# Kernel tuning notes

Measured on AMD Instinct MI355X. Metric: run time of the kernel, lower is better.

Reference implementation:

```python
import jax, jax.numpy as jnp
import numpy as np

HIDDEN = 4096
N_HEADS = 32
N_KV_HEADS = 8
HEAD_DIM = HIDDEN // N_HEADS  # 128
N_GROUPS = N_HEADS // N_KV_HEADS  # 4
ROPE_THETA = 10000.0
BSZ, SEQ = 2, 2048


def rotate_half(x):
    x1 = x[..., : x.shape[-1] // 2]
    x2 = x[..., x.shape[-1] // 2 :]
    return jnp.concatenate((-x2, x1), axis=-1)


def rope_tables(seq_len, head_dim, theta):
    inv_freq = 1.0 / theta ** (jnp.arange(0, head_dim, 2, dtype=jnp.float32) / head_dim)
    t = jnp.arange(seq_len, dtype=jnp.float32)
    freqs = jnp.einsum('i,j->ij', t, inv_freq)          # [S, head_dim/2]
    emb = jnp.concatenate((freqs, freqs), axis=-1)       # [S, head_dim]
    return jnp.cos(emb), jnp.sin(emb)


def setup_inputs() -> dict:
    key = jax.random.key(0)
    ks = jax.random.split(key, 5)
    hidden_states = jax.random.normal(ks[0], (BSZ, SEQ, HIDDEN), dtype=jnp.float32)
    # causal additive mask [B, 1, Q, K]
    causal = jnp.tril(jnp.ones((SEQ, SEQ), dtype=bool))
    attention_mask = jnp.where(causal, 0.0, -1e9).astype(jnp.float32)
    attention_mask = jnp.broadcast_to(attention_mask[None, None], (BSZ, 1, SEQ, SEQ))
    position_ids = jnp.broadcast_to(jnp.arange(SEQ, dtype=jnp.int32)[None, :], (BSZ, SEQ))
    sc = 1.0 / np.sqrt(HIDDEN)
    Wq = jax.random.normal(ks[1], (HIDDEN, N_HEADS * HEAD_DIM), dtype=jnp.float32) * sc
    Wk = jax.random.normal(ks[2], (HIDDEN, N_KV_HEADS * HEAD_DIM), dtype=jnp.float32) * sc
    Wv = jax.random.normal(ks[3], (HIDDEN, N_KV_HEADS * HEAD_DIM), dtype=jnp.float32) * sc
    Wo = jax.random.normal(ks[4], (N_HEADS * HEAD_DIM, HIDDEN), dtype=jnp.float32) * sc
    return {
        'hidden_states': hidden_states,
        'attention_mask': attention_mask,
        'position_ids': position_ids,
        'Wq': Wq, 'Wk': Wk, 'Wv': Wv, 'Wo': Wo,
    }


def reference(hidden_states, attention_mask, position_ids, Wq, Wk, Wv, Wo):
    bsz, q_len, _ = hidden_states.shape
    # QKV projections
    q = (hidden_states @ Wq).reshape(bsz, q_len, N_HEADS, HEAD_DIM).swapaxes(1, 2)       # [B,H,S,D]
    k = (hidden_states @ Wk).reshape(bsz, q_len, N_KV_HEADS, HEAD_DIM).swapaxes(1, 2)    # [B,Hkv,S,D]
    v = (hidden_states @ Wv).reshape(bsz, q_len, N_KV_HEADS, HEAD_DIM).swapaxes(1, 2)    # [B,Hkv,S,D]
    # RoPE
    cos_t, sin_t = rope_tables(q_len, HEAD_DIM, ROPE_THETA)
    cos = jnp.take(cos_t, position_ids, axis=0)[:, None]  # [B,1,S,D]
    sin = jnp.take(sin_t, position_ids, axis=0)[:, None]
    q = q * cos + rotate_half(q) * sin
    k = k * cos + rotate_half(k) * sin
    # GQA attention via grouped einsum (equivalent to repeat_kv, without materializing repeats)
    qg = q.reshape(bsz, N_KV_HEADS, N_GROUPS, q_len, HEAD_DIM)
    scores = jnp.einsum('bhgqd,bhkd->bhgqk', qg, k) / jnp.sqrt(jnp.float32(HEAD_DIM))
    scores = scores + attention_mask[:, :, None]  # broadcast mask over (kv_head, group)
    probs = jax.nn.softmax(scores.astype(jnp.float32), axis=-1).astype(hidden_states.dtype)
    out = jnp.einsum('bhgqk,bhkd->bhgqd', probs, v)
    out = out.reshape(bsz, N_HEADS, q_len, HEAD_DIM).swapaxes(1, 2).reshape(bsz, q_len, HIDDEN)
    return out @ Wo
```

## Files before the change

### kernel.cpp

```cpp
#include <hip/hip_runtime.h>
#include <hip/hip_bf16.h>
#include <cstdint>

#define HIDDEN 4096
#define NH 32
#define NKV 8
#define HD 128
#define SEQ 2048
#define BSZ 2
#define QKVN 6144
#define QKVLD 6144

using bf16x8 = __attribute__((ext_vector_type(8))) short;
using f32x4  = __attribute__((ext_vector_type(4))) float;

__device__ __forceinline__ ushort f2bf(float f) {
  union { float f; uint32_t u; } v; v.f = f;
  uint32_t r = (v.u + 0x7FFFu + ((v.u >> 16) & 1u)) >> 16;
  return (ushort)r;
}
__device__ __forceinline__ float bf2f(ushort s) {
  union { uint32_t u; float f; } v; v.u = ((uint32_t)s) << 16;
  return v.f;
}

__device__ __forceinline__ void gload_lds16(const void* g, void* l) {
  __builtin_amdgcn_global_load_lds(
      (const __attribute__((address_space(1))) void*)g,
      (__attribute__((address_space(3))) void*)l, 16, 0, 0);
}

__global__ __launch_bounds__(256)
void cvt_bf16_kernel(const float* __restrict__ X, ushort* __restrict__ Xb, int n8) {
  int t = blockIdx.x * 256 + threadIdx.x;
  if (t >= n8) return;
  size_t i = (size_t)t * 8;
  float4 a = *(const float4*)(X + i);
  float4 b = *(const float4*)(X + i + 4);
  uint4 p;
  p.x = (uint)f2bf(a.x) | ((uint)f2bf(a.y) << 16);
  p.y = (uint)f2bf(a.z) | ((uint)f2bf(a.w) << 16);
  p.z = (uint)f2bf(b.x) | ((uint)f2bf(b.y) << 16);
  p.w = (uint)f2bf(b.z) | ((uint)f2bf(b.w) << 16);
  *(uint4*)(Xb + i) = p;
}

__global__ __launch_bounds__(256)
void transpose_bf16_kernel(const float* __restrict__ W, ushort* __restrict__ WT,
                           int K, int N) {
  __shared__ ushort tile[32][33];
  const int k0 = blockIdx.y * 32, n0 = blockIdx.x * 32;
  const int tx = threadIdx.x & 31, ty = threadIdx.x >> 5;
  for (int i = 0; i < 4; ++i) {
    int k = ty + i * 8;
    tile[k][tx] = f2bf(W[(size_t)(k0 + k) * N + n0 + tx]);
  }
  __syncthreads();
  for (int i = 0; i < 4; ++i) {
    int n = ty + i * 8;
    WT[(size_t)(n0 + n) * K + k0 + tx] = tile[tx][n];
  }
}

__global__ __launch_bounds__(256)
void transpose_v_kernel(const ushort* __restrict__ Vsrc, ushort* __restrict__ VtG) {
  __shared__ ushort tile[32][33];
  const int slice = blockIdx.z;
  const int b = slice >> 3, kh = slice & 7;
  const int s0 = blockIdx.x * 32, d0 = blockIdx.y * 32;
  const int tx = threadIdx.x & 31, ty = threadIdx.x >> 5;
  const ushort* src = Vsrc + ((size_t)(b * SEQ) + s0) * QKVLD + kh * HD + d0;
  for (int i = 0; i < 4; ++i) {
    int s = ty + i * 8;
    tile[s][tx] = src[(size_t)s * QKVLD + tx];
  }
  __syncthreads();
  ushort* dst = VtG + ((size_t)slice * HD + d0) * SEQ + s0;
  for (int i = 0; i < 4; ++i) {
    int d = ty + i * 8;
    dst[(size_t)d * SEQ + tx] = tile[tx][d];
  }
}

template<int OUT_BF16>
__global__ __launch_bounds__(512, 2)
void gemm8p_kernel(const ushort* __restrict__ A, const ushort* __restrict__ BT,
                   void* __restrict__ Cp, int M, int N, int K) {
  extern __shared__ ushort lds[];
  const int tid = threadIdx.x, lane = tid & 63, wave = tid >> 6;
  const int l15 = lane & 15, l4 = lane >> 4;
  const int wr = wave >> 2, wc = wave & 3;

  const int mt = M >> 8, nt = N >> 8, nwg = mt * nt;
  const int swq = nwg >> 3, swr = nwg & 7;
  const int xcd = blockIdx.x & 7, lo = blockIdx.x >> 3;
  const int wg = (xcd < swr ? xcd * (swq + 1) : swr * (swq + 1) + (xcd - swr) * swq) + lo;
  const int m0 = (wg % mt) << 8;
  const int n0 = (wg / mt) << 8;

  ushort* LA[2][2];
  ushort* LB[2][2];
#pragma unroll
  for (int b_ = 0; b_ < 2; ++b_)
#pragma unroll
    for (int s_ = 0; s_ < 2; ++s_) {
      LA[b_][s_] = lds + ((b_ * 2 + 0) * 2 + s_) * 8192;
      LB[b_][s_] = lds + ((b_ * 2 + 1) * 2 + s_) * 8192;
    }

  const ushort* Abase = A + (size_t)m0 * K;
  const ushort* Bbase = BT + (size_t)n0 * K;

  const int srow0 = tid >> 2;
  const int scol8 = (((tid & 3) ^ ((srow0 >> 1) & 3)) << 3);

  const int swb  = (l4 ^ ((l15 >> 1) & 3)) << 3;
  const int aoff = (wr * 128 + l15) * 32 + swb;
  const int boff = (wc * 64 + l15) * 32 + swb;

  f32x4 acc[8][4] = {};
  bf16x8 a[8];
  bf16x8 b[4];

#define STAGE(buf, ks, kt, part)                                              \
  do {                                                                        \
    const size_t gc_ = (size_t)(kt) * 64 + (ks) * 32 + scol8;                 \
    const int rw_ = srow0 + (part) * 128;                                     \
    const int dst_ = ((part) * 512 + tid) * 8;                                \
    gload_lds16(Abase + (size_t)rw_ * K + gc_, &LA[buf][ks][dst_]);           \
    gload_lds16(Bbase + (size_t)rw_ * K + gc_, &LB[buf][ks][dst_]);           \
  } while (0)

#define MFMA_ __builtin_amdgcn_mfma_f32_16x16x32_bf16

#define PHASE_EVEN(buf, ks, sb, sk, skt)                                      \
  {                                                                           \
    _Pragma("unroll") for (int m_ = 0; m_ < 8; ++m_)                          \
      a[m_] = *(const bf16x8*)&LA[buf][ks][aoff + m_ * 512];                  \
    b[0] = *(const bf16x8*)&LB[buf][ks][boff];                                \
    b[1] = *(const bf16x8*)&LB[buf][ks][boff + 512];                          \
    STAGE(sb, sk, skt, 0);                                                    \
    asm volatile("s_barrier" ::: "memory");                                   \
    __builtin_amdgcn_s_setprio(1);                                            \
    _Pragma("unroll") for (int m_ = 0; m_ < 8; ++m_) {                        \
      acc[m_][0] = MFMA_(a[m_], b[0], acc[m_][0], 0, 0, 0);                   \
      acc[m_][1] = MFMA_(a[m_], b[1], acc[m_][1], 0, 0, 0);                   \
    }                                                                         \
    __builtin_amdgcn_s_setprio(0);                                            \
    asm volatile("s_barrier" ::: "memory");                                   \
  }

#define PHASE_ODD(buf, ks, sb, sk, skt)                                       \
  {                                                                           \
    b[2] = *(const bf16x8*)&LB[buf][ks][boff + 1024];                         \
    b[3] = *(const bf16x8*)&LB[buf][ks][boff + 1536];                         \
    STAGE(sb, sk, skt, 1);                                                    \
    asm volatile("s_barrier" ::: "memory");                                   \
    __builtin_amdgcn_s_setprio(1);                                            \
    _Pragma("unroll") for (int m_ = 0; m_ < 8; ++m_) {                        \
      acc[m_][2] = MFMA_(a[m_], b[2], acc[m_][2], 0, 0, 0);                   \
      acc[m_][3] = MFMA_(a[m_], b[3], acc[m_][3], 0, 0, 0);                   \
    }                                                                         \
    __builtin_amdgcn_s_setprio(0);                                            \
    asm volatile("s_waitcnt vmcnt(8)");                                       \
    asm volatile("s_barrier" ::: "memory");                                   \
  }

  const int NT = K >> 6;

  STAGE(0, 0, 0, 0); STAGE(0, 0, 0, 1);
  STAGE(0, 1, 0, 0); STAGE(0, 1, 0, 1);
  STAGE(1, 0, 1, 0); STAGE(1, 0, 1, 1);
  asm volatile("s_waitcnt vmcnt(8)");
  asm volatile("s_barrier" ::: "memory");

  for (int i = 0; i < (NT >> 1); ++i) {
    const int kt0 = 2 * i;
    const int ktA = (kt0 + 2 < NT) ? kt0 + 2 : NT - 1;
    const int ktB = (kt0 + 3 < NT) ? kt0 + 3 : NT - 1;
    PHASE_EVEN(0, 0, 1, 1, kt0 + 1)
    PHASE_ODD (0, 0, 1, 1, kt0 + 1)
    PHASE_EVEN(0, 1, 0, 0, ktA)
    PHASE_ODD (0, 1, 0, 0, ktA)
    PHASE_EVEN(1, 0, 0, 1, ktA)
    PHASE_ODD (1, 0, 0, 1, ktA)
    PHASE_EVEN(1, 1, 1, 0, ktB)
    PHASE_ODD (1, 1, 1, 0, ktB)
  }
#undef PHASE_EVEN
#undef PHASE_ODD
#undef STAGE

  const int crow0 = m0 + wr * 128 + l4 * 4;
  const int ccol0 = n0 + wc * 64 + l15;
#pragma unroll
  for (int m_ = 0; m_ < 8; ++m_)
#pragma unroll
    for (int n_ = 0; n_ < 4; ++n_)
#pragma unroll
      for (int r_ = 0; r_ < 4; ++r_) {
        const size_t row = crow0 + m_ * 16 + r_;
        const int col = ccol0 + n_ * 16;
        const float val = acc[m_][n_][r_];
        if (OUT_BF16) ((ushort*)Cp)[row * N + col] = f2bf(val);
        else          ((float*)Cp)[row * N + col]  = val;
      }
}

__global__ __launch_bounds__(256)
void rope_kernel(ushort* buf, const int* __restrict__ pos_ids, int nh, int ld, int total) {
  int t = blockIdx.x * 256 + threadIdx.x;
  if (t >= total) return;
  int j = t & 63;
  int rest = t >> 6;
  int h = rest % nh;
  int bs = rest / nh;
  float pos = (float)pos_ids[bs];
  float inv = exp2f(-(float)j * (13.287712379549449f / 64.0f));
  float ang = pos * inv;
  float c = cosf(ang), s = sinf(ang);
  ushort* p = buf + (size_t)bs * ld + h * HD + j;
  float x1 = bf2f(p[0]), x2 = bf2f(p[64]);
  p[0]  = f2bf(x1 * c - x2 * s);
  p[64] = f2bf(x2 * c + x1 * s);
}

__global__ __launch_bounds__(256)
void attn_kernel(const ushort* __restrict__ Q, const ushort* __restrict__ K0,
                 const ushort* __restrict__ VtG, ushort* __restrict__ AO) {
  __shared__ ushort Ks[64 * 128];
  __shared__ ushort Vs[2][128 * 64];
  __shared__ ushort Ps[4][32 * 72];

  const int raw  = blockIdx.x;
  const int kh   = raw & 7;
  const int rest = raw >> 3;
  const int qt   = 63 - (rest & 63);
  const int b    = rest >> 6;
  const int q0   = qt * 32;

  const int tid = threadIdx.x, lane = tid & 63, wave = tid >> 6;
  const int l15 = lane & 15, l4 = lane >> 4;
  const int h = kh * 4 + wave;
  const float SCL2 = 0.1275173110f;

  const size_t bS = (size_t)b * SEQ;
  const ushort* Kb = K0 + bS * QKVLD + kh * HD;
  const ushort* Vb = VtG + (size_t)(b * NKV + kh) * HD * SEQ;

  const int vrow = lane >> 3;
  const int vslot = lane & 7;

  bf16x8 qf[2][4];
#pragma unroll
  for (int mi = 0; mi < 2; ++mi) {
    const ushort* qp = Q + (bS + q0 + mi * 16 + l15) * QKVLD + h * HD + l4 * 8;
#pragma unroll
    for (int kk = 0; kk < 4; ++kk) qf[mi][kk] = *(const bf16x8*)(qp + kk * 32);
  }

  float mrow[2][4], denom[2][4];
#pragma unroll
  for (int mi = 0; mi < 2; ++mi)
#pragma unroll
    for (int r = 0; r < 4; ++r) { mrow[mi][r] = -1e30f; denom[mi][r] = 0.0f; }
  f32x4 accO[2][8] = {};

  const int nt = qt / 2 + 1;

  {
#pragma unroll
    for (int c = 0; c < 4; ++c) {
      const int j = wave * 4 + c;
      const int row = j * 4 + l4;
      const int chunk = l15 ^ (row & 7);
      gload_lds16(Kb + (size_t)row * QKVLD + chunk * 8, &Ks[j * 512 + lane * 8]);
    }
#pragma unroll
    for (int c = 0; c < 4; ++c) {
      const int j = wave * 4 + c;
      const int d = j * 8 + vrow;
      const int chunk = vslot ^ (d & 7);
      gload_lds16(Vb + (size_t)d * SEQ + chunk * 8, &Vs[0][j * 512 + lane * 8]);
    }
  }
  __syncthreads();

  for (int t = 0; t < nt; ++t) {
    const int k0 = t * 64;
    const int cur = t & 1;
    const bool mask_tile = (t == nt - 1);
    const bool pf = (t + 1 < nt);

    f32x4 accS[2][4] = {};
    __builtin_amdgcn_s_setprio(1);
#pragma unroll
    for (int kk = 0; kk < 4; ++kk) {
#pragma unroll
      for (int ni = 0; ni < 4; ++ni) {
        bf16x8 kf = *(const bf16x8*)&Ks[(ni * 16 + l15) * 128 +
                                        (((kk * 4 + l4) ^ (l15 & 7)) << 3)];
        accS[0][ni] = __builtin_amdgcn_mfma_f32_16x16x32_bf16(qf[0][kk], kf, accS[0][ni], 0, 0, 0);
        accS[1][ni] = __builtin_amdgcn_mfma_f32_16x16x32_bf16(qf[1][kk], kf, accS[1][ni], 0, 0, 0);
      }
    }
    __builtin_amdgcn_s_setprio(0);
    __syncthreads();

    if (pf) {
      const int kn = k0 + 64;
#pragma unroll
      for (int c = 0; c < 4; ++c) {
        const int j = wave * 4 + c;
        const int row = j * 4 + l4;
        const int chunk = l15 ^ (row & 7);
        gload_lds16(Kb + (size_t)(kn + row) * QKVLD + chunk * 8, &Ks[j * 512 + lane * 8]);
      }
#pragma unroll
      for (int c = 0; c < 4; ++c) {
        const int j = wave * 4 + c;
        const int d = j * 8 + vrow;
        const int chunk = vslot ^ (d & 7);
        gload_lds16(Vb + (size_t)d * SEQ + kn + chunk * 8,
                    &Vs[cur ^ 1][j * 512 + lane * 8]);
      }
    }

    float pmax[2][4];
#pragma unroll
    for (int mi = 0; mi < 2; ++mi)
#pragma unroll
      for (int r = 0; r < 4; ++r) {
        float mx = -3e38f;
#pragma unroll
        for (int ni = 0; ni < 4; ++ni) {
          float x = accS[mi][ni][r] * SCL2;
          if (mask_tile) {
            int kq = k0 + ni * 16 + l15;
            int qq = q0 + mi * 16 + l4 * 4 + r;
            if (kq > qq) x = -1e30f;
          }
          accS[mi][ni][r] = x;
          mx = fmaxf(mx, x);
        }
        pmax[mi][r] = mx;
      }

    bool ok = true;
#pragma unroll
    for (int mi = 0; mi < 2; ++mi)
#pragma unroll
      for (int r = 0; r < 4; ++r)
        ok = ok && (pmax[mi][r] - mrow[mi][r] <= 8.0f);

    if (__all(ok)) {
#pragma unroll
      for (int mi = 0; mi < 2; ++mi)
#pragma unroll
        for (int r = 0; r < 4; ++r) {
          const float mn = mrow[mi][r];
          float s = 0.0f;
#pragma unroll
          for (int ni = 0; ni < 4; ++ni) {
            float p = exp2f(accS[mi][ni][r] - mn);
            accS[mi][ni][r] = p;
            s += p;
          }
          denom[mi][r] += s;
        }
    } else {
#pragma unroll
      for (int d = 1; d < 16; d <<= 1)
#pragma unroll
        for (int mi = 0; mi < 2; ++mi)
#pragma unroll
          for (int r = 0; r < 4; ++r)
            pmax[mi][r] = fmaxf(pmax[mi][r], __shfl_xor(pmax[mi][r], d));
#pragma unroll
      for (int mi = 0; mi < 2; ++mi)
#pragma unroll
        for (int r = 0; r < 4; ++r) {
          const float mn = fmaxf(mrow[mi][r], pmax[mi][r]);
          const float alpha = exp2f(mrow[mi][r] - mn);
          mrow[mi][r] = mn;
          float s = 0.0f;
#pragma unroll
          for (int ni = 0; ni < 4; ++ni) {
            float p = exp2f(accS[mi][ni][r] - mn);
            accS[mi][ni][r] = p;
            s += p;
          }
          denom[mi][r] = denom[mi][r] * alpha + s;
#pragma unroll
          for (int db = 0; db < 8; ++db) accO[mi][db][r] *= alpha;
        }
    }

#pragma unroll
    for (int mi = 0; mi < 2; ++mi)
#pragma unroll
      for (int ni = 0; ni < 4; ++ni)
#pragma unroll
        for (int r = 0; r < 4; ++r)
          Ps[wave][(mi * 16 + l4 * 4 + r) * 72 + ni * 16 + l15] = f2bf(accS[mi][ni][r]);

    __builtin_amdgcn_s_setprio(1);
#pragma unroll
    for (int kk = 0; kk < 2; ++kk) {
      bf16x8 pa[2];
#pragma unroll
      for (int mi = 0; mi < 2; ++mi)
        pa[mi] = *(const bf16x8*)&Ps[wave][(mi * 16 + l15) * 72 + kk * 32 + l4 * 8];
#pragma unroll
      for (int db = 0; db < 8; ++db) {
        bf16x8 vb = *(const bf16x8*)&Vs[cur][(db * 16 + l15) * 64 +
                                            (((kk * 4 + l4) ^ (l15 & 7)) << 3)];
        accO[0][db] = __builtin_amdgcn_mfma_f32_16x16x32_bf16(pa[0], vb, accO[0][db], 0, 0, 0);
        accO[1][db] = __builtin_amdgcn_mfma_f32_16x16x32_bf16(pa[1], vb, accO[1][db], 0, 0, 0);
      }
    }
    __builtin_amdgcn_s_setprio(0);

    __syncthreads();
  }

#pragma unroll
  for (int d = 1; d < 16; d <<= 1)
#pragma unroll
    for (int mi = 0; mi < 2; ++mi)
#pragma unroll
      for (int r = 0; r < 4; ++r)
        denom[mi][r] += __shfl_xor(denom[mi][r], d);

#pragma unroll
  for (int mi = 0; mi < 2; ++mi)
#pragma unroll
    for (int db = 0; db < 8; ++db)
#pragma unroll
      for (int r = 0; r < 4; ++r) {
        int q = q0 + mi * 16 + l4 * 4 + r;
        int col = h * HD + db * 16 + l15;
        AO[(bS + q) * HIDDEN + col] = f2bf(accO[mi][db][r] / denom[mi][r]);
      }
}

extern "C" void kernel_launch(void* const* d_in, const int* in_sizes, int n_in,
                              void* d_out, int out_size, void* d_ws, size_t ws_size,
                              hipStream_t stream) {
  (void)in_sizes; (void)n_in; (void)out_size; (void)ws_size;
  const float* X   = (const float*)d_in[0];
  const int*   pos = (const int*)d_in[2];
  const float* Wq  = (const float*)d_in[3];
  const float* Wk  = (const float*)d_in[4];
  const float* Wv  = (const float*)d_in[5];
  const float* Wo  = (const float*)d_in[6];

  char* ws = (char*)d_ws;
  ushort* Xb    = (ushort*)(ws);
  ushort* QKV   = (ushort*)(ws + 33554432);
  ushort* BTqkv = (ushort*)(ws + 83886080);
  ushort* WoT   = (ushort*)(ws + 134217728);
  ushort* AO    = Xb;
  ushort* VtG   = BTqkv;

  const int M = BSZ * SEQ;
  dim3 blk(256);

  hipFuncSetAttribute((const void*)gemm8p_kernel<1>,
                      hipFuncAttributeMaxDynamicSharedMemorySize, 131072);
  hipFuncSetAttribute((const void*)gemm8p_kernel<0>,
                      hipFuncAttributeMaxDynamicSharedMemorySize, 131072);

  cvt_bf16_kernel<<<dim3((M * HIDDEN / 8 + 255) / 256), blk, 0, stream>>>(X, Xb, M * HIDDEN / 8);
  transpose_bf16_kernel<<<dim3(HIDDEN / 32, HIDDEN / 32), blk, 0, stream>>>(Wq, BTqkv, HIDDEN, HIDDEN);
  transpose_bf16_kernel<<<dim3((NKV * HD) / 32, HIDDEN / 32), blk, 0, stream>>>(
      Wk, BTqkv + (size_t)HIDDEN * HIDDEN, HIDDEN, NKV * HD);
  transpose_bf16_kernel<<<dim3((NKV * HD) / 32, HIDDEN / 32), blk, 0, stream>>>(
      Wv, BTqkv + (size_t)(HIDDEN + NKV * HD) * HIDDEN, HIDDEN, NKV * HD);
  transpose_bf16_kernel<<<dim3(HIDDEN / 32, HIDDEN / 32), blk, 0, stream>>>(Wo, WoT, HIDDEN, HIDDEN);

  gemm8p_kernel<1><<<dim3((M / 256) * (QKVN / 256)), dim3(512), 131072, stream>>>(
      Xb, BTqkv, QKV, M, QKVN, HIDDEN);

  rope_kernel<<<dim3((M * NH * 64) / 256), blk, 0, stream>>>(QKV, pos, NH, QKVLD, M * NH * 64);
  rope_kernel<<<dim3((M * NKV * 64) / 256), blk, 0, stream>>>(QKV + HIDDEN, pos, NKV, QKVLD, M * NKV * 64);
  transpose_v_kernel<<<dim3(SEQ / 32, HD / 32, BSZ * NKV), blk, 0, stream>>>(
      QKV + HIDDEN + NKV * HD, VtG);

  attn_kernel<<<dim3(8 * 64 * BSZ), blk, 0, stream>>>(QKV, QKV + HIDDEN, VtG, AO);

  gemm8p_kernel<0><<<dim3((M / 256) * (HIDDEN / 256)), dim3(512), 131072, stream>>>(
      AO, WoT, d_out, M, HIDDEN, HIDDEN);
}
```

Baseline: 639.1 us.

## Restructure attention to 32x32 MFMA with register-resident P and larger query blocks

Rewrites the attention kernel so each 512-thread block processes 256 queries of one head, with eight waves of 32 queries sharing each staged K/V tile. It switches to 32x32x16 MFMA and computes S transposed, so P can be packed to bf16 and rearranged with permlane32 swaps directly in registers instead of going through LDS. It also folds the softmax scale into Q during RoPE and skips fully masked tiles per wave. The aim is fewer K/V loads per query, no P round-trip through LDS, and less scaling work. The cost is more register pressure per thread, fewer blocks in the grid, and idle waves on the causal diagonal tiles.

```diff
diff --git a/kernel.cpp b/kernel.cpp
--- a/kernel.cpp
+++ b/kernel.cpp
@@ -13,6 +13,7 @@
 
 using bf16x8 = __attribute__((ext_vector_type(8))) short;
 using f32x4  = __attribute__((ext_vector_type(4))) float;
+using f32x16 = __attribute__((ext_vector_type(16))) float;
 
 __device__ __forceinline__ ushort f2bf(float f) {
   union { float f; uint32_t u; } v; v.f = f;
@@ -22,6 +23,15 @@
 __device__ __forceinline__ float bf2f(ushort s) {
   union { uint32_t u; float f; } v; v.u = ((uint32_t)s) << 16;
   return v.f;
+}
+
+__device__ __forceinline__ uint32_t cvtpk(float lo, float hi) {
+  uint32_t r;
+  asm("v_cvt_pk_bf16_f32 %0, %1, %2" : "=v"(r) : "v"(lo), "v"(hi));
+  return r;
+}
+__device__ __forceinline__ void pl32swap(uint32_t& a, uint32_t& b) {
+  asm("v_permlane32_swap_b32 %0, %1" : "+v"(a), "+v"(b));
 }
 
 __device__ __forceinline__ void gload_lds16(const void* g, void* l) {
@@ -208,7 +218,8 @@
 }
 
 __global__ __launch_bounds__(256)
-void rope_kernel(ushort* buf, const int* __restrict__ pos_ids, int nh, int ld, int total) {
+void rope_kernel(ushort* buf, const int* __restrict__ pos_ids, int nh, int ld,
+                 int total, float oscale) {
   int t = blockIdx.x * 256 + threadIdx.x;
   if (t >= total) return;
   int j = t & 63;
@@ -218,230 +229,174 @@
   float pos = (float)pos_ids[bs];
   float inv = exp2f(-(float)j * (13.287712379549449f / 64.0f));
   float ang = pos * inv;
-  float c = cosf(ang), s = sinf(ang);
+  float c = cosf(ang) * oscale, s = sinf(ang) * oscale;
   ushort* p = buf + (size_t)bs * ld + h * HD + j;
   float x1 = bf2f(p[0]), x2 = bf2f(p[64]);
   p[0]  = f2bf(x1 * c - x2 * s);
   p[64] = f2bf(x2 * c + x1 * s);
 }
 
-__global__ __launch_bounds__(256)
+__global__ __launch_bounds__(512)
 void attn_kernel(const ushort* __restrict__ Q, const ushort* __restrict__ K0,
                  const ushort* __restrict__ VtG, ushort* __restrict__ AO) {
   __shared__ ushort Ks[64 * 128];
   __shared__ ushort Vs[2][128 * 64];
-  __shared__ ushort Ps[4][32 * 72];
-
-  const int raw  = blockIdx.x;
-  const int kh   = raw & 7;
-  const int rest = raw >> 3;
-  const int qt   = 63 - (rest & 63);
-  const int b    = rest >> 6;
-  const int q0   = qt * 32;
-
-  const int tid = threadIdx.x, lane = tid & 63, wave = tid >> 6;
-  const int l15 = lane & 15, l4 = lane >> 4;
-  const int h = kh * 4 + wave;
-  const float SCL2 = 0.1275173110f;
+
+  const int bid = blockIdx.x;
+  const int kh  = bid & 7;
+  const int r2  = bid >> 3;
+  const int qtB = 7 - (r2 & 7);
+  const int hq  = (r2 >> 3) & 3;
+  const int b   = r2 >> 5;
+  const int h   = kh * 4 + hq;
+  const int q0b = qtB * 256;
+
+  const int tid = threadIdx.x, lane = tid & 63, w = tid >> 6;
+  const int l31 = lane & 31, hi = lane >> 5;
+  const int q0w = q0b + w * 32;
 
   const size_t bS = (size_t)b * SEQ;
   const ushort* Kb = K0 + bS * QKVLD + kh * HD;
   const ushort* Vb = VtG + (size_t)(b * NKV + kh) * HD * SEQ;
 
-  const int vrow = lane >> 3;
-  const int vslot = lane & 7;
-
-  bf16x8 qf[2][4];
-#pragma unroll
-  for (int mi = 0; mi < 2; ++mi) {
-    const ushort* qp = Q + (bS + q0 + mi * 16 + l15) * QKVLD + h * HD + l4 * 8;
-#pragma unroll
-    for (int kk = 0; kk < 4; ++kk) qf[mi][kk] = *(const bf16x8*)(qp + kk * 32);
-  }
-
-  float mrow[2][4], denom[2][4];
-#pragma unroll
-  for (int mi = 0; mi < 2; ++mi)
-#pragma unroll
-    for (int r = 0; r < 4; ++r) { mrow[mi][r] = -1e30f; denom[mi][r] = 0.0f; }
-  f32x4 accO[2][8] = {};
-
-  const int nt = qt / 2 + 1;
-
+  bf16x8 qf[8];
   {
-#pragma unroll
-    for (int c = 0; c < 4; ++c) {
-      const int j = wave * 4 + c;
-      const int row = j * 4 + l4;
-      const int chunk = l15 ^ (row & 7);
-      gload_lds16(Kb + (size_t)row * QKVLD + chunk * 8, &Ks[j * 512 + lane * 8]);
-    }
-#pragma unroll
-    for (int c = 0; c < 4; ++c) {
-      const int j = wave * 4 + c;
-      const int d = j * 8 + vrow;
-      const int chunk = vslot ^ (d & 7);
-      gload_lds16(Vb + (size_t)d * SEQ + chunk * 8, &Vs[0][j * 512 + lane * 8]);
-    }
-  }
+    const ushort* qp = Q + (bS + q0w + l31) * QKVLD + h * HD + hi * 8;
+#pragma unroll
+    for (int ds = 0; ds < 8; ++ds) qf[ds] = *(const bf16x8*)(qp + ds * 16);
+  }
+
+  f32x16 accO[4] = {};
+  float mrow = -1e30f, denom = 0.0f;
+
+  const int nt = qtB * 4 + 4;
+
+  const int j0 = 2 * w, j1 = 2 * w + 1;
+  const int kl4 = lane >> 4, ks15 = lane & 15;
+  const int vl3 = lane >> 3, vs7 = lane & 7;
+  const int kswz = lane & 15;
+  const int vswz = lane & 7;
+
+#define KSTAGE(jj, kk0) { const int k_ = (jj) * 4 + kl4;                       \
+    gload_lds16(Kb + (size_t)((kk0) + k_) * QKVLD + ((ks15 ^ (k_ & 15)) << 3), \
+                &Ks[(jj) * 512 + lane * 8]); }
+#define VSTAGE(jj, bb, kk0) { const int d_ = (jj) * 8 + vl3;                   \
+    gload_lds16(Vb + (size_t)d_ * SEQ + (kk0) + ((vs7 ^ (d_ & 7)) << 3),       \
+                &Vs[bb][(jj) * 512 + lane * 8]); }
+
+  KSTAGE(j0, 0) KSTAGE(j1, 0) VSTAGE(j0, 0, 0) VSTAGE(j1, 0, 0)
   __syncthreads();
 
   for (int t = 0; t < nt; ++t) {
     const int k0 = t * 64;
     const int cur = t & 1;
-    const bool mask_tile = (t == nt - 1);
     const bool pf = (t + 1 < nt);
-
-    f32x4 accS[2][4] = {};
-    __builtin_amdgcn_s_setprio(1);
-#pragma unroll
-    for (int kk = 0; kk < 4; ++kk) {
-#pragma unroll
-      for (int ni = 0; ni < 4; ++ni) {
-        bf16x8 kf = *(const bf16x8*)&Ks[(ni * 16 + l15) * 128 +
-                                        (((kk * 4 + l4) ^ (l15 & 7)) << 3)];
-        accS[0][ni] = __builtin_amdgcn_mfma_f32_16x16x32_bf16(qf[0][kk], kf, accS[0][ni], 0, 0, 0);
-        accS[1][ni] = __builtin_amdgcn_mfma_f32_16x16x32_bf16(qf[1][kk], kf, accS[1][ni], 0, 0, 0);
-      }
+    const bool skip = (k0 > q0w + 31);
+
+    f32x16 s0 = {}, s1 = {};
+    if (!skip) {
+      __builtin_amdgcn_s_setprio(1);
+#pragma unroll
+      for (int ds = 0; ds < 8; ++ds) {
+        const int so = ((ds * 2 + hi) ^ kswz) << 3;
+        bf16x8 kf0 = *(const bf16x8*)&Ks[l31 * 128 + so];
+        bf16x8 kf1 = *(const bf16x8*)&Ks[(32 + l31) * 128 + so];
+        s0 = __builtin_amdgcn_mfma_f32_32x32x16_bf16(kf0, qf[ds], s0, 0, 0, 0);
+        s1 = __builtin_amdgcn_mfma_f32_32x32x16_bf16(kf1, qf[ds], s1, 0, 0, 0);
+      }
+      __builtin_amdgcn_s_setprio(0);
     }
-    __builtin_amdgcn_s_setprio(0);
     __syncthreads();
 
     if (pf) {
       const int kn = k0 + 64;
-#pragma unroll
-      for (int c = 0; c < 4; ++c) {
-        const int j = wave * 4 + c;
-        const int row = j * 4 + l4;
-        const int chunk = l15 ^ (row & 7);
-        gload_lds16(Kb + (size_t)(kn + row) * QKVLD + chunk * 8, &Ks[j * 512 + lane * 8]);
-      }
-#pragma unroll
-      for (int c = 0; c < 4; ++c) {
-        const int j = wave * 4 + c;
-        const int d = j * 8 + vrow;
-        const int chunk = vslot ^ (d & 7);
-        gload_lds16(Vb + (size_t)d * SEQ + kn + chunk * 8,
-                    &Vs[cur ^ 1][j * 512 + lane * 8]);
-      }
+      KSTAGE(j0, kn) KSTAGE(j1, kn) VSTAGE(j0, cur ^ 1, kn) VSTAGE(j1, cur ^ 1, kn)
     }
 
-    float pmax[2][4];
-#pragma unroll
-    for (int mi = 0; mi < 2; ++mi)
-#pragma unroll
-      for (int r = 0; r < 4; ++r) {
-        float mx = -3e38f;
-#pragma unroll
-        for (int ni = 0; ni < 4; ++ni) {
-          float x = accS[mi][ni][r] * SCL2;
-          if (mask_tile) {
-            int kq = k0 + ni * 16 + l15;
-            int qq = q0 + mi * 16 + l4 * 4 + r;
-            if (kq > qq) x = -1e30f;
-          }
-          accS[mi][ni][r] = x;
-          mx = fmaxf(mx, x);
+    if (!skip) {
+      if (k0 + 63 > q0w) {
+        const int qrel = q0w + l31 - k0;
+#pragma unroll
+        for (int r = 0; r < 16; ++r) {
+          const int kc = (r & 3) + 8 * (r >> 2) + 4 * hi;
+          if (kc > qrel)      s0[r] = -1e30f;
+          if (kc + 32 > qrel) s1[r] = -1e30f;
         }
-        pmax[mi][r] = mx;
-      }
-
-    bool ok = true;
-#pragma unroll
-    for (int mi = 0; mi < 2; ++mi)
-#pragma unroll
-      for (int r = 0; r < 4; ++r)
-        ok = ok && (pmax[mi][r] - mrow[mi][r] <= 8.0f);
-
-    if (__all(ok)) {
-#pragma unroll
-      for (int mi = 0; mi < 2; ++mi)
-#pragma unroll
-        for (int r = 0; r < 4; ++r) {
-          const float mn = mrow[mi][r];
-          float s = 0.0f;
-#pragma unroll
-          for (int ni = 0; ni < 4; ++ni) {
-            float p = exp2f(accS[mi][ni][r] - mn);
-            accS[mi][ni][r] = p;
-            s += p;
-          }
-          denom[mi][r] += s;
+      }
+      float pm = s0[0];
+#pragma unroll
+      for (int r = 1; r < 16; ++r) pm = fmaxf(pm, s0[r]);
+#pragma unroll
+      for (int r = 0; r < 16; ++r) pm = fmaxf(pm, s1[r]);
+
+      if (!__all(pm - mrow <= 8.0f)) {
+        pm = fmaxf(pm, __shfl_xor(pm, 32));
+        const float mn = fmaxf(mrow, pm);
+        const float alpha = exp2f(mrow - mn);
+        mrow = mn;
+        denom *= alpha;
+#pragma unroll
+        for (int du = 0; du < 4; ++du)
+#pragma unroll
+          for (int r = 0; r < 16; ++r) accO[du][r] *= alpha;
+      }
+      float ssum = 0.0f;
+#pragma unroll
+      for (int r = 0; r < 16; ++r) { float p = exp2f(s0[r] - mrow); s0[r] = p; ssum += p; }
+#pragma unroll
+      for (int r = 0; r < 16; ++r) { float p = exp2f(s1[r] - mrow); s1[r] = p; ssum += p; }
+      denom += ssum;
+
+      uint32_t paw[4][4];
+      {
+        uint32_t p0 = cvtpk(s0[0], s0[1]),   p1 = cvtpk(s0[2], s0[3]);
+        uint32_t p2 = cvtpk(s0[4], s0[5]),   p3 = cvtpk(s0[6], s0[7]);
+        uint32_t p4 = cvtpk(s0[8], s0[9]),   p5 = cvtpk(s0[10], s0[11]);
+        uint32_t p6 = cvtpk(s0[12], s0[13]), p7 = cvtpk(s0[14], s0[15]);
+        pl32swap(p0, p2); pl32swap(p1, p3); pl32swap(p4, p6); pl32swap(p5, p7);
+        paw[0][0] = p0; paw[0][1] = p1; paw[0][2] = p2; paw[0][3] = p3;
+        paw[1][0] = p4; paw[1][1] = p5; paw[1][2] = p6; paw[1][3] = p7;
+      }
+      {
+        uint32_t p0 = cvtpk(s1[0], s1[1]),   p1 = cvtpk(s1[2], s1[3]);
+        uint32_t p2 = cvtpk(s1[4], s1[5]),   p3 = cvtpk(s1[6], s1[7]);
+        uint32_t p4 = cvtpk(s1[8], s1[9]),   p5 = cvtpk(s1[10], s1[11]);
+        uint32_t p6 = cvtpk(s1[12], s1[13]), p7 = cvtpk(s1[14], s1[15]);
+        pl32swap(p0, p2); pl32swap(p1, p3); pl32swap(p4, p6); pl32swap(p5, p7);
+        paw[2][0] = p0; paw[2][1] = p1; paw[2][2] = p2; paw[2][3] = p3;
+        paw[3][0] = p4; paw[3][1] = p5; paw[3][2] = p6; paw[3][3] = p7;
+      }
+
+      __builtin_amdgcn_s_setprio(1);
+#pragma unroll
+      for (int du = 0; du < 4; ++du) {
+#pragma unroll
+        for (int ks = 0; ks < 4; ++ks) {
+          const int so = ((ks * 2 + hi) ^ vswz) << 3;
+          bf16x8 vf = *(const bf16x8*)&Vs[cur][(du * 32 + l31) * 64 + so];
+          bf16x8 pb = *(const bf16x8*)&paw[ks][0];
+          accO[du] = __builtin_amdgcn_mfma_f32_32x32x16_bf16(vf, pb, accO[du], 0, 0, 0);
         }
-    } else {
-#pragma unroll
-      for (int d = 1; d < 16; d <<= 1)
-#pragma unroll
-        for (int mi = 0; mi < 2; ++mi)
-#pragma unroll
-          for (int r = 0; r < 4; ++r)
-            pmax[mi][r] = fmaxf(pmax[mi][r], __shfl_xor(pmax[mi][r], d));
-#pragma unroll
-      for (int mi = 0; mi < 2; ++mi)
-#pragma unroll
-        for (int r = 0; r < 4; ++r) {
-          const float mn = fmaxf(mrow[mi][r], pmax[mi][r]);
-          const float alpha = exp2f(mrow[mi][r] - mn);
-          mrow[mi][r] = mn;
-          float s = 0.0f;
-#pragma unroll
-          for (int ni = 0; ni < 4; ++ni) {
-            float p = exp2f(accS[mi][ni][r] - mn);
-            accS[mi][ni][r] = p;
-            s += p;
-          }
-          denom[mi][r] = denom[mi][r] * alpha + s;
-#pragma unroll
-          for (int db = 0; db < 8; ++db) accO[mi][db][r] *= alpha;
-        }
+      }
+      __builtin_amdgcn_s_setprio(0);
     }
-
-#pragma unroll
-    for (int mi = 0; mi < 2; ++mi)
-#pragma unroll
-      for (int ni = 0; ni < 4; ++ni)
-#pragma unroll
-        for (int r = 0; r < 4; ++r)
-          Ps[wave][(mi * 16 + l4 * 4 + r) * 72 + ni * 16 + l15] = f2bf(accS[mi][ni][r]);
-
-    __builtin_amdgcn_s_setprio(1);
-#pragma unroll
-    for (int kk = 0; kk < 2; ++kk) {
-      bf16x8 pa[2];
-#pragma unroll
-      for (int mi = 0; mi < 2; ++mi)
-        pa[mi] = *(const bf16x8*)&Ps[wave][(mi * 16 + l15) * 72 + kk * 32 + l4 * 8];
-#pragma unroll
-      for (int db = 0; db < 8; ++db) {
-        bf16x8 vb = *(const bf16x8*)&Vs[cur][(db * 16 + l15) * 64 +
-                                            (((kk * 4 + l4) ^ (l15 & 7)) << 3)];
-        accO[0][db] = __builtin_amdgcn_mfma_f32_16x16x32_bf16(pa[0], vb, accO[0][db], 0, 0, 0);
-        accO[1][db] = __builtin_amdgcn_mfma_f32_16x16x32_bf16(pa[1], vb, accO[1][db], 0, 0, 0);
-      }
+    __syncthreads();
+  }
+#undef KSTAGE
+#undef VSTAGE
+
+  denom += __shfl_xor(denom, 32);
+  const float inv = 1.0f / denom;
+  ushort* op = AO + (bS + q0w + l31) * HIDDEN + h * HD + hi * 4;
+#pragma unroll
+  for (int du = 0; du < 4; ++du)
+#pragma unroll
+    for (int g = 0; g < 4; ++g) {
+      uint2 u;
+      u.x = cvtpk(accO[du][4 * g + 0] * inv, accO[du][4 * g + 1] * inv);
+      u.y = cvtpk(accO[du][4 * g + 2] * inv, accO[du][4 * g + 3] * inv);
+      *(uint2*)(op + du * 32 + g * 8) = u;
     }
-    __builtin_amdgcn_s_setprio(0);
-
-    __syncthreads();
-  }
-
-#pragma unroll
-  for (int d = 1; d < 16; d <<= 1)
-#pragma unroll
-    for (int mi = 0; mi < 2; ++mi)
-#pragma unroll
-      for (int r = 0; r < 4; ++r)
-        denom[mi][r] += __shfl_xor(denom[mi][r], d);
-
-#pragma unroll
-  for (int mi = 0; mi < 2; ++mi)
-#pragma unroll
-    for (int db = 0; db < 8; ++db)
-#pragma unroll
-      for (int r = 0; r < 4; ++r) {
-        int q = q0 + mi * 16 + l4 * 4 + r;
-        int col = h * HD + db * 16 + l15;
-        AO[(bS + q) * HIDDEN + col] = f2bf(accO[mi][db][r] / denom[mi][r]);
-      }
 }
 
 extern "C" void kernel_launch(void* const* d_in, const int* in_sizes, int n_in,
@@ -482,12 +437,14 @@
   gemm8p_kernel<1><<<dim3((M / 256) * (QKVN / 256)), dim3(512), 131072, stream>>>(
       Xb, BTqkv, QKV, M, QKVN, HIDDEN);
 
-  rope_kernel<<<dim3((M * NH * 64) / 256), blk, 0, stream>>>(QKV, pos, NH, QKVLD, M * NH * 64);
-  rope_kernel<<<dim3((M * NKV * 64) / 256), blk, 0, stream>>>(QKV + HIDDEN, pos, NKV, QKVLD, M * NKV * 64);
+  rope_kernel<<<dim3((M * NH * 64) / 256), blk, 0, stream>>>(
+      QKV, pos, NH, QKVLD, M * NH * 64, 0.12751731f);
+  rope_kernel<<<dim3((M * NKV * 64) / 256), blk, 0, stream>>>(
+      QKV + HIDDEN, pos, NKV, QKVLD, M * NKV * 64, 1.0f);
   transpose_v_kernel<<<dim3(SEQ / 32, HD / 32, BSZ * NKV), blk, 0, stream>>>(
       QKV + HIDDEN + NKV * HD, VtG);
 
-  attn_kernel<<<dim3(8 * 64 * BSZ), blk, 0, stream>>>(QKV, QKV + HIDDEN, VtG, AO);
+  attn_kernel<<<dim3(512), dim3(512), 0, stream>>>(QKV, QKV + HIDDEN, VtG, AO);
 
   gemm8p_kernel<0><<<dim3((M / 256) * (HIDDEN / 256)), dim3(512), 131072, stream>>>(
       AO, WoT, d_out, M, HIDDEN, HIDDEN);
```

After: 598.0 us. 6.4% less time.
